# Performance work log

Hardware: AMD Instinct MI355X
Metric: run time of the kernel (lower is better)

Reference implementation:

```python
import jax, jax.numpy as jnp
import numpy as np

HEADS, BATCH, SEQ, CDIM = 8, 4, 2048, 32
WINDOW = 10

def setup_inputs() -> dict:
    key = jax.random.key(0)
    k1, k2, k3, k4 = jax.random.split(key, 4)
    shp = (HEADS, BATCH, SEQ, CDIM)
    return {
        'Q': jax.random.normal(k1, shp, dtype=jnp.float32),
        'K': jax.random.normal(k2, shp, dtype=jnp.float32),
        'V': jax.random.normal(k3, shp, dtype=jnp.float32),
        'G': jax.random.normal(k4, shp, dtype=jnp.float32),
        'seqMask': jnp.zeros((BATCH, SEQ), dtype=bool),  # no padded positions
    }

def reference(Q, K, V, G, seqMask):
    # Q,K,V,G: [h, n, s, c]; seqMask: [n, s] bool (True = masked key position)
    scale = 1.0 / jnp.sqrt(jnp.asarray(CDIM, dtype=Q.dtype))
    A = jnp.einsum('hnsi,hnti->hnst', Q, K) * scale  # [h,n,s,t]
    # padding mask on key axis
    A = jnp.where(seqMask[None, :, None, :], -jnp.inf, A)
    # local band mask |s-t| <= WINDOW (torch scatter construction clamps to
    # row bounds, which is equivalent to the plain band)
    idx = jnp.arange(SEQ)
    band = jnp.abs(idx[:, None] - idx[None, :]) <= WINDOW  # [s,t]
    A = jnp.where(band[None, None, :, :], A, -jnp.inf)
    A = jax.nn.softmax(A, axis=-1)
    # gated AV fusion: out[n,s,h,i] = sum_t A[h,n,s,t] V[h,n,t,i] * G[h,n,s,i]
    out = jnp.einsum('hnst,hnti,hnsi->nshi', A, V, G)
    return out
```

## Files before the change

### kernel.cpp

```cpp
#include <hip/hip_runtime.h>
#include <hip/hip_bf16.h>
#include <math.h>

#define HEADS 8
#define BATCH 4
#define SEQ 2048
#define CDIM 32
#define WINDOW 10

#define RPB 64
#define KROWS 96
#define VROWS 112

typedef float f32x4 __attribute__((ext_vector_type(4)));
typedef short s16x8 __attribute__((ext_vector_type(8)));
#define MFMA16 __builtin_amdgcn_mfma_f32_16x16x32_bf16

union BF8 { s16x8 v; __hip_bfloat162 h[4]; };
union U32 { __hip_bfloat162 h; unsigned u; };
union U4  { unsigned u[4]; s16x8 v; };
union US  { unsigned short s[8]; s16x8 v; };

__global__ __launch_bounds__(256) void lwin_attn_kernel(
    const float* __restrict__ Q, const float* __restrict__ K,
    const float* __restrict__ V, const float* __restrict__ G,
    const unsigned char* __restrict__ seqMask, float* __restrict__ out)
{
    __shared__ short K_s[KROWS * 32];
    __shared__ short V_s[VROWS * 32];
    __shared__ unsigned long long bm_lds[2];

    const int d = blockIdx.x;
    const int b = (d & 7) * 128 + (d >> 3);

    const int hn = b >> 5;
    const int s0 = (b & 31) * RPB;
    const int n  = hn & 3;
    const int h  = hn >> 2;
    const int base_hn = hn * SEQ * CDIM;

    const int tid  = threadIdx.x;
    const int w    = tid >> 6;
    const int lane = tid & 63;
    const int q    = lane & 15;
    const int g    = lane >> 4;

    if (w < 2) {
        const int i  = w * 64 + lane;
        const int t  = s0 - 16 + i;
        const int tc = min(max(t, 0), SEQ - 1);
        const bool inval = (t < 0) || (t >= SEQ) || (seqMask[n * SEQ + tc] != 0);
        const unsigned long long bw = __ballot(inval);
        if (lane == 0) bm_lds[w] = bw;
    }

#pragma unroll
    for (int it = 0; it < 4; ++it) {
        const int task = tid + it * 256;
        if (task < 384) {
            const int i = task >> 2, o = task & 3;
            const int t  = s0 - 16 + i;
            const int tc = min(max(t, 0), SEQ - 1);
            const float4 f0 = *(const float4*)&K[base_hn + tc * 32 + 8 * o];
            const float4 f1 = *(const float4*)&K[base_hn + tc * 32 + 8 * o + 4];
            BF8 u;
            u.h[0] = __float22bfloat162_rn(make_float2(f0.x, f0.y));
            u.h[1] = __float22bfloat162_rn(make_float2(f0.z, f0.w));
            u.h[2] = __float22bfloat162_rn(make_float2(f1.x, f1.y));
            u.h[3] = __float22bfloat162_rn(make_float2(f1.z, f1.w));
            *(s16x8*)&K_s[i * 32 + 8 * o] = u.v;
        } else if (task < 384 + 448) {
            const int vt = task - 384;
            const int i = vt >> 2, o = vt & 3;
            const int t  = s0 - 16 + i;
            const int tc = min(max(t, 0), SEQ - 1);
            const float4 f0 = *(const float4*)&V[base_hn + tc * 32 + 8 * o];
            const float4 f1 = *(const float4*)&V[base_hn + tc * 32 + 8 * o + 4];
            BF8 u;
            u.h[0] = __float22bfloat162_rn(make_float2(f0.x, f0.y));
            u.h[1] = __float22bfloat162_rn(make_float2(f0.z, f0.w));
            u.h[2] = __float22bfloat162_rn(make_float2(f1.x, f1.y));
            u.h[3] = __float22bfloat162_rn(make_float2(f1.z, f1.w));
            *(s16x8*)&V_s[i * 32 + 8 * o] = u.v;
        }
    }

    const int sw   = s0 + 16 * w;
    const int rowq = hn * SEQ + sw + q;
    const float sc = 0.17677669529663687f * 1.4426950408889634f;
    const float4 q0 = *(const float4*)&Q[rowq * 32 + 8 * g];
    const float4 q1 = *(const float4*)&Q[rowq * 32 + 8 * g + 4];
    BF8 bq;
    bq.h[0] = __float22bfloat162_rn(make_float2(q0.x * sc, q0.y * sc));
    bq.h[1] = __float22bfloat162_rn(make_float2(q0.z * sc, q0.w * sc));
    bq.h[2] = __float22bfloat162_rn(make_float2(q1.x * sc, q1.y * sc));
    bq.h[3] = __float22bfloat162_rn(make_float2(q1.z * sc, q1.w * sc));

    __syncthreads();

    f32x4 S[3];
#pragma unroll
    for (int blk = 0; blk < 3; ++blk) {
        const s16x8 ak = *(const s16x8*)&K_s[(16 * w + 16 * blk + q) * 32 + 8 * g];
        S[blk] = MFMA16(ak, bq.v, (f32x4){0.f, 0.f, 0.f, 0.f}, 0, 0, 0);
    }

    const unsigned long long bm0 = bm_lds[0], bm1 = bm_lds[1];
    bool vld[3][4];
    float mx = -1e30f;
#pragma unroll
    for (int blk = 0; blk < 3; ++blk)
#pragma unroll
        for (int r = 0; r < 4; ++r) {
            const int j = 16 * blk + 4 * g + r;
            const int i = 16 * w + j;
            const int rel = j - 16 - q;
            const bool band_ok = (rel >= -WINDOW) && (rel <= WINDOW);
            const bool bm_ok =
                !(((i < 64) ? (bm0 >> i) : (bm1 >> (i - 64))) & 1ULL);
            vld[blk][r] = band_ok && bm_ok;
            mx = fmaxf(mx, vld[blk][r] ? S[blk][r] : -1e30f);
        }
    mx = fmaxf(mx, __shfl_xor(mx, 16));
    mx = fmaxf(mx, __shfl_xor(mx, 32));

    float P[3][4];
    float sm = 0.f;
#pragma unroll
    for (int blk = 0; blk < 3; ++blk)
#pragma unroll
        for (int r = 0; r < 4; ++r) {
            const float e = vld[blk][r] ? __builtin_amdgcn_exp2f(S[blk][r] - mx) : 0.f;
            P[blk][r] = e;
            sm += e;
        }
    sm += __shfl_xor(sm, 16);
    sm += __shfl_xor(sm, 32);
    const float inv = 1.0f / sm;

    unsigned pk[3][2];
#pragma unroll
    for (int blk = 0; blk < 3; ++blk) {
        U32 a, b2;
        a.h  = __float22bfloat162_rn(make_float2(P[blk][0] * inv, P[blk][1] * inv));
        b2.h = __float22bfloat162_rn(make_float2(P[blk][2] * inv, P[blk][3] * inv));
        pk[blk][0] = a.u;
        pk[blk][1] = b2.u;
    }

    U4 A1, A2;
#pragma unroll
    for (int j = 0; j < 4; ++j) {
        const int srcl = q + 16 * (2 * (g & 1) + (j >> 1));
        const unsigned x0 = __shfl(pk[0][j & 1], srcl);
        const unsigned x1 = __shfl(pk[1][j & 1], srcl);
        const unsigned x2 = __shfl(pk[2][j & 1], srcl);
        A1.u[j] = (g >> 1) ? x1 : x0;
        A2.u[j] = (g < 2) ? x2 : 0u;
    }

    f32x4 O0 = {0.f, 0.f, 0.f, 0.f}, O1 = {0.f, 0.f, 0.f, 0.f};
    const unsigned short* __restrict__ vs = (const unsigned short*)V_s;
#pragma unroll
    for (int sb = 0; sb < 2; ++sb) {
        US b0, b1;
#pragma unroll
        for (int j = 0; j < 8; ++j) {
            const int vrow = 16 * w + 32 * sb + 8 * g + j;
            b0.s[j] = vs[vrow * 32 + q];
            b1.s[j] = vs[vrow * 32 + q + 16];
        }
        const s16x8 Af = (sb == 0) ? A1.v : A2.v;
        O0 = MFMA16(Af, b0.v, O0, 0, 0, 0);
        O1 = MFMA16(Af, b1.v, O1, 0, 0, 0);
    }

#pragma unroll
    for (int p = 0; p < 2; ++p)
#pragma unroll
        for (int r = 0; r < 4; ++r) {
            const int orow = sw + 4 * g + r;
            const int ch   = q + 16 * p;
            const float gv = G[(hn * SEQ + orow) * 32 + ch];
            const float ov = (p == 0) ? O0[r] : O1[r];
            out[((n * SEQ + orow) * HEADS + h) * 32 + ch] = ov * gv;
        }
}

extern "C" void kernel_launch(void* const* d_in, const int* in_sizes, int n_in,
                              void* d_out, int out_size, void* d_ws, size_t ws_size,
                              hipStream_t stream) {
    const float* Q = (const float*)d_in[0];
    const float* K = (const float*)d_in[1];
    const float* V = (const float*)d_in[2];
    const float* G = (const float*)d_in[3];
    const unsigned char* seqMask = (const unsigned char*)d_in[4];
    float* out = (float*)d_out;

    const int blocks = HEADS * BATCH * (SEQ / RPB);
    lwin_attn_kernel<<<blocks, 256, 0, stream>>>(Q, K, V, G, seqMask, out);
}
```

Baseline: 12.58 us.

## Compute transposed PV MFMA with interleaved V layout and vectorized gated output

Stores V in shared memory as packed bf16 pairs (channel c with c+16) using a padded stride, and swaps the operands of the PV MFMA so the probability fragment from QK^T can be used directly, without cross-lane shuffles. The output is then laid out per row, so G loads and output stores become float4 vectors. The band and padding mask becomes a single 64-bit bitmask, and softmax normalization moves after the MFMA. This targets the shuffle overhead, scalar 16-bit LDS gathers and strided scalar global stores, at the cost of byte-permute instructions and a more intricate layout whose correctness depends on careful index mapping.

```diff
diff --git a/kernel.cpp b/kernel.cpp
--- a/kernel.cpp
+++ b/kernel.cpp
@@ -11,6 +11,7 @@
 #define RPB 64
 #define KROWS 96
 #define VROWS 112
+#define VSTR 20
 
 typedef float f32x4 __attribute__((ext_vector_type(4)));
 typedef short s16x8 __attribute__((ext_vector_type(8)));
@@ -19,7 +20,6 @@
 union BF8 { s16x8 v; __hip_bfloat162 h[4]; };
 union U32 { __hip_bfloat162 h; unsigned u; };
 union U4  { unsigned u[4]; s16x8 v; };
-union US  { unsigned short s[8]; s16x8 v; };
 
 __global__ __launch_bounds__(256) void lwin_attn_kernel(
     const float* __restrict__ Q, const float* __restrict__ K,
@@ -27,7 +27,7 @@
     const unsigned char* __restrict__ seqMask, float* __restrict__ out)
 {
     __shared__ short K_s[KROWS * 32];
-    __shared__ short V_s[VROWS * 32];
+    __shared__ unsigned V_s[VROWS * VSTR];
     __shared__ unsigned long long bm_lds[2];
 
     const int d = blockIdx.x;
@@ -74,14 +74,15 @@
             const int i = vt >> 2, o = vt & 3;
             const int t  = s0 - 16 + i;
             const int tc = min(max(t, 0), SEQ - 1);
-            const float4 f0 = *(const float4*)&V[base_hn + tc * 32 + 8 * o];
-            const float4 f1 = *(const float4*)&V[base_hn + tc * 32 + 8 * o + 4];
-            BF8 u;
-            u.h[0] = __float22bfloat162_rn(make_float2(f0.x, f0.y));
-            u.h[1] = __float22bfloat162_rn(make_float2(f0.z, f0.w));
-            u.h[2] = __float22bfloat162_rn(make_float2(f1.x, f1.y));
-            u.h[3] = __float22bfloat162_rn(make_float2(f1.z, f1.w));
-            *(s16x8*)&V_s[i * 32 + 8 * o] = u.v;
+            const float4 f0 = *(const float4*)&V[base_hn + tc * 32 + 4 * o];
+            const float4 f1 = *(const float4*)&V[base_hn + tc * 32 + 16 + 4 * o];
+            U32 w0, w1, w2, w3;
+            w0.h = __float22bfloat162_rn(make_float2(f0.x, f1.x));
+            w1.h = __float22bfloat162_rn(make_float2(f0.y, f1.y));
+            w2.h = __float22bfloat162_rn(make_float2(f0.z, f1.z));
+            w3.h = __float22bfloat162_rn(make_float2(f0.w, f1.w));
+            uint4 pk4 = make_uint4(w0.u, w1.u, w2.u, w3.u);
+            *(uint4*)&V_s[i * VSTR + 4 * o] = pk4;
         }
     }
 
@@ -106,85 +107,85 @@
     }
 
     const unsigned long long bm0 = bm_lds[0], bm1 = bm_lds[1];
-    bool vld[3][4];
+    const unsigned long long mI = (bm0 >> (16 * w)) | ((bm1 << (63 - 16 * w)) << 1);
+    const unsigned long long vm = (((1ULL << 21) - 1) << (q + 6)) & ~mI;
+
+    float X[3][4];
     float mx = -1e30f;
 #pragma unroll
     for (int blk = 0; blk < 3; ++blk)
 #pragma unroll
         for (int r = 0; r < 4; ++r) {
             const int j = 16 * blk + 4 * g + r;
-            const int i = 16 * w + j;
-            const int rel = j - 16 - q;
-            const bool band_ok = (rel >= -WINDOW) && (rel <= WINDOW);
-            const bool bm_ok =
-                !(((i < 64) ? (bm0 >> i) : (bm1 >> (i - 64))) & 1ULL);
-            vld[blk][r] = band_ok && bm_ok;
-            mx = fmaxf(mx, vld[blk][r] ? S[blk][r] : -1e30f);
+            const float x = ((vm >> j) & 1ULL) ? S[blk][r] : -1e30f;
+            X[blk][r] = x;
+            mx = fmaxf(mx, x);
         }
     mx = fmaxf(mx, __shfl_xor(mx, 16));
     mx = fmaxf(mx, __shfl_xor(mx, 32));
 
-    float P[3][4];
     float sm = 0.f;
 #pragma unroll
     for (int blk = 0; blk < 3; ++blk)
 #pragma unroll
         for (int r = 0; r < 4; ++r) {
-            const float e = vld[blk][r] ? __builtin_amdgcn_exp2f(S[blk][r] - mx) : 0.f;
-            P[blk][r] = e;
+            const float e = __builtin_amdgcn_exp2f(X[blk][r] - mx);
+            X[blk][r] = e;
             sm += e;
         }
     sm += __shfl_xor(sm, 16);
     sm += __shfl_xor(sm, 32);
-    const float inv = 1.0f / sm;
 
     unsigned pk[3][2];
 #pragma unroll
     for (int blk = 0; blk < 3; ++blk) {
         U32 a, b2;
-        a.h  = __float22bfloat162_rn(make_float2(P[blk][0] * inv, P[blk][1] * inv));
-        b2.h = __float22bfloat162_rn(make_float2(P[blk][2] * inv, P[blk][3] * inv));
+        a.h  = __float22bfloat162_rn(make_float2(X[blk][0], X[blk][1]));
+        b2.h = __float22bfloat162_rn(make_float2(X[blk][2], X[blk][3]));
         pk[blk][0] = a.u;
         pk[blk][1] = b2.u;
     }
 
-    U4 A1, A2;
-#pragma unroll
-    for (int j = 0; j < 4; ++j) {
-        const int srcl = q + 16 * (2 * (g & 1) + (j >> 1));
-        const unsigned x0 = __shfl(pk[0][j & 1], srcl);
-        const unsigned x1 = __shfl(pk[1][j & 1], srcl);
-        const unsigned x2 = __shfl(pk[2][j & 1], srcl);
-        A1.u[j] = (g >> 1) ? x1 : x0;
-        A2.u[j] = (g < 2) ? x2 : 0u;
-    }
-
     f32x4 O0 = {0.f, 0.f, 0.f, 0.f}, O1 = {0.f, 0.f, 0.f, 0.f};
-    const unsigned short* __restrict__ vs = (const unsigned short*)V_s;
 #pragma unroll
     for (int sb = 0; sb < 2; ++sb) {
-        US b0, b1;
-#pragma unroll
-        for (int j = 0; j < 8; ++j) {
-            const int vrow = 16 * w + 32 * sb + 8 * g + j;
-            b0.s[j] = vs[vrow * 32 + q];
-            b1.s[j] = vs[vrow * 32 + q + 16];
-        }
-        const s16x8 Af = (sb == 0) ? A1.v : A2.v;
-        O0 = MFMA16(Af, b0.v, O0, 0, 0, 0);
-        O1 = MFMA16(Af, b1.v, O1, 0, 0, 0);
-    }
-
-#pragma unroll
-    for (int p = 0; p < 2; ++p)
-#pragma unroll
-        for (int r = 0; r < 4; ++r) {
-            const int orow = sw + 4 * g + r;
-            const int ch   = q + 16 * p;
-            const float gv = G[(hn * SEQ + orow) * 32 + ch];
-            const float ov = (p == 0) ? O0[r] : O1[r];
-            out[((n * SEQ + orow) * HEADS + h) * 32 + ch] = ov * gv;
-        }
+        const int R = 16 * w + 32 * sb;
+        unsigned r0[4], r1[4];
+#pragma unroll
+        for (int jj = 0; jj < 4; ++jj) {
+            r0[jj] = V_s[(R + 4 * g + jj) * VSTR + q];
+            r1[jj] = V_s[(R + 16 + 4 * g + jj) * VSTR + q];
+        }
+        U4 A0, A1v;
+        A0.u[0]  = __builtin_amdgcn_perm(r0[1], r0[0], 0x05040100u);
+        A0.u[1]  = __builtin_amdgcn_perm(r0[3], r0[2], 0x05040100u);
+        A0.u[2]  = __builtin_amdgcn_perm(r1[1], r1[0], 0x05040100u);
+        A0.u[3]  = __builtin_amdgcn_perm(r1[3], r1[2], 0x05040100u);
+        A1v.u[0] = __builtin_amdgcn_perm(r0[1], r0[0], 0x07060302u);
+        A1v.u[1] = __builtin_amdgcn_perm(r0[3], r0[2], 0x07060302u);
+        A1v.u[2] = __builtin_amdgcn_perm(r1[1], r1[0], 0x07060302u);
+        A1v.u[3] = __builtin_amdgcn_perm(r1[3], r1[2], 0x07060302u);
+        U4 Bp;
+        if (sb == 0) { Bp.u[0] = pk[0][0]; Bp.u[1] = pk[0][1];
+                       Bp.u[2] = pk[1][0]; Bp.u[3] = pk[1][1]; }
+        else         { Bp.u[0] = pk[2][0]; Bp.u[1] = pk[2][1];
+                       Bp.u[2] = 0u;       Bp.u[3] = 0u; }
+        O0 = MFMA16(A0.v,  Bp.v, O0, 0, 0, 0);
+        O1 = MFMA16(A1v.v, Bp.v, O1, 0, 0, 0);
+    }
+
+    const float invq = 1.0f / sm;
+    const int orow = sw + q;
+    const float4 g0 = *(const float4*)&G[(hn * SEQ + orow) * 32 + 4 * g];
+    const float4 g1 = *(const float4*)&G[(hn * SEQ + orow) * 32 + 16 + 4 * g];
+    float4 o0, o1;
+    o0.x = O0[0] * invq * g0.x;  o0.y = O0[1] * invq * g0.y;
+    o0.z = O0[2] * invq * g0.z;  o0.w = O0[3] * invq * g0.w;
+    o1.x = O1[0] * invq * g1.x;  o1.y = O1[1] * invq * g1.y;
+    o1.z = O1[2] * invq * g1.z;  o1.w = O1[3] * invq * g1.w;
+    float* obase = &out[((n * SEQ + orow) * HEADS + h) * 32];
+    *(float4*)&obase[4 * g]      = o0;
+    *(float4*)&obase[16 + 4 * g] = o1;
 }
 
 extern "C" void kernel_launch(void* const* d_in, const int* in_sizes, int n_in,
```

Result: faster. 11.96 us (-5.0%).
